# Kernel optimization log

Measured on AMD Instinct MI355X. Metric: run time of the kernel, lower is better.

Reference implementation:

```python
import jax, jax.numpy as jnp
import numpy as np

N = 50000      # nodes
E = 800000     # edges
IN = 128       # in_channels
HID = 128      # hidden_channels
OUT = 2        # out_channels (edge classes)
HEADS = 8      # EGConv default num_heads
BASES = 4      # EGConv default num_bases
FH = HID // HEADS  # per-head feature dim = 16


def _egconv(x, Wb, Wc, bc, b, row, col, norm, n):
    """One EGConv layer (aggregators=['symnorm']), self-loops already in row/col/norm.
    Wb: [in, BASES*FH] basis projection (no bias).
    Wc: [in, HEADS*BASES], bc: combination weights linear.
    b : [HID] output bias.
    """
    bases = x @ Wb                                            # [n, BASES*FH]
    msg = bases[row] * norm[:, None]                          # gather + symnorm scale
    agg = jax.ops.segment_sum(msg, col, num_segments=n)       # scatter-add -> [n, BASES*FH]
    w = (x @ Wc + bc).reshape(n, HEADS, BASES)                # per-node combination weights
    out = jnp.einsum('nhb,nbf->nhf', w, agg.reshape(n, BASES, FH))
    return out.reshape(n, HEADS * FH) + b


def setup_inputs() -> dict:
    key = jax.random.key(0)
    ks = jax.random.split(key, 12)
    s = 0.05
    inp = {
        'x': jax.random.normal(ks[0], (N, IN), jnp.float32),
        'edge_index': jax.random.randint(ks[1], (2, E), 0, N, jnp.int64),
        # conv1
        'Wb1': jax.random.normal(ks[2], (IN, BASES * FH), jnp.float32) * s,
        'Wc1': jax.random.normal(ks[3], (IN, HEADS * BASES), jnp.float32) * s,
        'bc1': jnp.zeros((HEADS * BASES,), jnp.float32),
        'b1': jnp.zeros((HID,), jnp.float32),
        # conv2
        'Wb2': jax.random.normal(ks[4], (HID, BASES * FH), jnp.float32) * s,
        'Wc2': jax.random.normal(ks[5], (HID, HEADS * BASES), jnp.float32) * s,
        'bc2': jnp.zeros((HEADS * BASES,), jnp.float32),
        'b2': jnp.zeros((HID,), jnp.float32),
        # edge classifier
        'Wcls': jax.random.normal(ks[6], (2 * HID, OUT), jnp.float32) * s,
        'bcls': jnp.zeros((OUT,), jnp.float32),
    }
    return inp


def reference(x, edge_index, Wb1, Wc1, bc1, b1, Wb2, Wc2, bc2, b2, Wcls, bcls):
    n = x.shape[0]
    # add self loops (EGConv default add_self_loops=True) + gcn_norm symnorm weights
    sl = jnp.arange(n, dtype=edge_index.dtype)
    row = jnp.concatenate([edge_index[0], sl])
    col = jnp.concatenate([edge_index[1], sl])
    deg = jax.ops.segment_sum(jnp.ones(row.shape[0], x.dtype), col, num_segments=n)
    dis = jnp.where(deg > 0, deg, 1.0) ** -0.5
    dis = jnp.where(deg > 0, dis, 0.0)
    norm = dis[row] * dis[col]                                # symnorm edge weight

    h = jax.nn.relu(_egconv(x, Wb1, Wc1, bc1, b1, row, col, norm, n))
    h = _egconv(h, Wb2, Wc2, bc2, b2, row, col, norm, n)

    # edge classifier: gather endpoint embeddings of ORIGINAL edges, concat, linear
    e = jnp.concatenate([h[edge_index[0]], h[edge_index[1]]], axis=-1)  # [E, 2*HID]
    return e @ Wcls + bcls
```

## Files before the change

kernel.cpp:

```cpp
#include <hip/hip_runtime.h>
#include <hip/hip_fp16.h>

#define NN 50000
#define EE 800000
#define NB_E2 1563
#define WIN 6250
#define EPB 1024
#define NCHUNK 782

__global__ void k_count(const int* __restrict__ ei, int* cnt, int* __restrict__ rank) {
    int t = blockIdx.x * 256 + threadIdx.x;
    if (t < EE / 2) {
        int2 cc = *(const int2*)(ei + EE + 2 * t);
        int r0 = atomicAdd(&cnt[cc.x], 1);
        int r1 = atomicAdd(&cnt[cc.y], 1);
        *(int2*)(rank + 2 * t) = make_int2(r0, r1);
    }
}

__global__ void k_scan1(const int* __restrict__ cnt, int* sloc, int* bsum,
                        float* dis, int n) {
    __shared__ int s[256];
    int tid = threadIdx.x;
    int i = blockIdx.x * 256 + tid;
    int v = (i < n) ? cnt[i] : 0;
    if (i < n) dis[i] = rsqrtf((float)v + 1.0f);
    s[tid] = v;
    __syncthreads();
    for (int off = 1; off < 256; off <<= 1) {
        int t2 = 0;
        if (tid >= off) t2 = s[tid - off];
        __syncthreads();
        if (tid >= off) s[tid] += t2;
        __syncthreads();
    }
    if (i < n) sloc[i] = s[tid] - v;
    if (tid == 255) bsum[blockIdx.x] = s[255];
}

__global__ void k_scan23(const int* __restrict__ sloc, const int* __restrict__ bsum,
                         const int* __restrict__ cnt, int2* sd, int* starts,
                         int n, int nb) {
    __shared__ int sb[256];
    int tid = threadIdx.x, b = blockIdx.x;
    int v = (tid < nb && tid < b) ? bsum[tid] : 0;
    sb[tid] = v;
    __syncthreads();
    for (int off = 128; off; off >>= 1) {
        if (tid < off) sb[tid] += sb[tid + off];
        __syncthreads();
    }
    int boff = sb[0];
    int i = b * 256 + tid;
    if (i < n) {
        int st = sloc[i] + boff;
        sd[i] = make_int2(st, cnt[i]);
        starts[i] = st;
    }
}

__global__ __launch_bounds__(256) void k_fill(
    const int* __restrict__ ei, const int* __restrict__ rank,
    const int* __restrict__ starts, int* __restrict__ csr)
{
    int w = blockIdx.x & 7;
    int chunk = blockIdx.x >> 3;
    int base = chunk * EPB + threadIdx.x * 4;
    int lo = w * WIN, hi = lo + WIN;
    if (base + 3 < EE) {
        int4 rr = *(const int4*)(ei + base);
        int4 cc = *(const int4*)(ei + EE + base);
        int4 rk = *(const int4*)(rank + base);
        if (cc.x >= lo && cc.x < hi) csr[starts[cc.x] + rk.x] = rr.x;
        if (cc.y >= lo && cc.y < hi) csr[starts[cc.y] + rk.y] = rr.y;
        if (cc.z >= lo && cc.z < hi) csr[starts[cc.z] + rk.z] = rr.z;
        if (cc.w >= lo && cc.w < hi) csr[starts[cc.w] + rk.w] = rr.w;
    } else {
        for (int e = 0; e < 4; e++) {
            int t = base + e;
            if (t < EE) {
                int c = ei[EE + t];
                if (c >= lo && c < hi) csr[starts[c] + rank[t]] = ei[t];
            }
        }
    }
}

__global__ __launch_bounds__(256) void k_gemm(
    const float* __restrict__ x, const float* __restrict__ Wb,
    const float* __restrict__ Wc, const float* __restrict__ bc,
    const float* __restrict__ dis,
    __half* __restrict__ bsh, float* __restrict__ wcomb, int n)
{
    __shared__ float xt[32 * 257];
    int tid = threadIdx.x;
    int grp = blockIdx.y;
    int row0 = blockIdx.x * 256;
    int row = row0 + tid;
    bool valid = row < n;

    const float* W = (grp < 2) ? (Wb + grp * 32) : Wc;
    const int ldw = (grp < 2) ? 64 : 32;

    float acc[32];
#pragma unroll
    for (int c = 0; c < 32; c++) acc[c] = 0.f;

    for (int s = 0; s < 4; s++) {
        int base_k = s * 32;
        float4 v[8];
#pragma unroll
        for (int i = 0; i < 8; i++) {
            int idx = i * 256 + tid;
            int r = idx >> 3;
            int k4 = idx & 7;
            int gr = row0 + r;
            v[i] = (gr < n) ? *(const float4*)(x + (size_t)gr * 128 + base_k + k4 * 4)
                            : make_float4(0.f, 0.f, 0.f, 0.f);
        }
        __syncthreads();
#pragma unroll
        for (int i = 0; i < 8; i++) {
            int idx = i * 256 + tid;
            int r = idx >> 3;
            int k4 = idx & 7;
            xt[(k4 * 4 + 0) * 257 + r] = v[i].x;
            xt[(k4 * 4 + 1) * 257 + r] = v[i].y;
            xt[(k4 * 4 + 2) * 257 + r] = v[i].z;
            xt[(k4 * 4 + 3) * 257 + r] = v[i].w;
        }
        __syncthreads();

        const float* Ws = W + base_k * ldw;
#pragma unroll 8
        for (int k = 0; k < 32; k++) {
            float xs = xt[k * 257 + tid];
            const float* wk = Ws + k * ldw;
#pragma unroll
            for (int c = 0; c < 32; c++) acc[c] = fmaf(xs, wk[c], acc[c]);
        }
    }

    if (!valid) return;
    if (grp < 2) {
        float d = dis[row];
        __half2 hh[16];
#pragma unroll
        for (int c = 0; c < 16; c++)
            hh[c] = __floats2half2_rn(acc[2 * c] * d, acc[2 * c + 1] * d);
        uint4* bo = (uint4*)(bsh + (size_t)row * 64 + grp * 32);
        const uint4* src = (const uint4*)hh;
#pragma unroll
        for (int c = 0; c < 4; c++) bo[c] = src[c];
    } else {
        float4* wo = (float4*)(wcomb + (size_t)row * 32);
#pragma unroll
        for (int c = 0; c < 8; c++)
            wo[c] = make_float4(acc[4*c] + bc[4*c], acc[4*c+1] + bc[4*c+1],
                                acc[4*c+2] + bc[4*c+2], acc[4*c+3] + bc[4*c+3]);
    }
}

template<int LAYER2>
__global__ __launch_bounds__(256) void k_agg(
    const int* __restrict__ csr, const int2* __restrict__ sd,
    const __half* __restrict__ bsh, const float* __restrict__ dis,
    const float* __restrict__ wcomb, const float* __restrict__ bias,
    float* __restrict__ h,
    const float* __restrict__ Wcls, const float* __restrict__ bcls,
    float* __restrict__ p, int n)
{
    int wid = (blockIdx.x * 256 + threadIdx.x) >> 6;
    int lane = threadIdx.x & 63;
    if (wid >= n) return;
    int2 s2 = sd[wid];
    int start = s2.x, deg = s2.y;
    int g = lane >> 4, q = lane & 15;

    const uint2* bsp = (const uint2*)bsh;
    float4 acc4 = make_float4(0.f, 0.f, 0.f, 0.f);
    if (g == 0) {
        uint2 v = bsp[(size_t)wid * 16 + q];
        float2 lo = __half22float2(*(const __half2*)&v.x);
        float2 hi = __half22float2(*(const __half2*)&v.y);
        acc4 = make_float4(lo.x, lo.y, hi.x, hi.y);
    }

    int j = 0;
    int ia = 0, ib = 0;
    if (8 <= deg) { ia = csr[start + g]; ib = csr[start + 4 + g]; }
    while (j + 8 <= deg) {
        int jn = j + 8;
        int na = 0, nb = 0;
        if (jn + 8 <= deg) { na = csr[start + jn + g]; nb = csr[start + jn + 4 + g]; }
        uint2 v0 = bsp[(size_t)ia * 16 + q];
        uint2 v1 = bsp[(size_t)ib * 16 + q];
        float2 l0 = __half22float2(*(const __half2*)&v0.x);
        float2 h0 = __half22float2(*(const __half2*)&v0.y);
        float2 l1 = __half22float2(*(const __half2*)&v1.x);
        float2 h1 = __half22float2(*(const __half2*)&v1.y);
        acc4.x += l0.x + l1.x;
        acc4.y += l0.y + l1.y;
        acc4.z += h0.x + h1.x;
        acc4.w += h0.y + h1.y;
        ia = na; ib = nb; j = jn;
    }
    int last = start + deg - 1;
    for (; j < deg; j += 4) {
        int idx = start + j + g;
        int r = csr[min(idx, last)];
        uint2 v = bsp[(size_t)r * 16 + q];
        float2 lo = __half22float2(*(const __half2*)&v.x);
        float2 hi = __half22float2(*(const __half2*)&v.y);
        float m = (j + g < deg) ? 1.f : 0.f;
        acc4.x = fmaf(lo.x, m, acc4.x);
        acc4.y = fmaf(lo.y, m, acc4.y);
        acc4.z = fmaf(hi.x, m, acc4.z);
        acc4.w = fmaf(hi.y, m, acc4.w);
    }

    acc4.x += __shfl_xor(acc4.x, 16, 64);
    acc4.y += __shfl_xor(acc4.y, 16, 64);
    acc4.z += __shfl_xor(acc4.z, 16, 64);
    acc4.w += __shfl_xor(acc4.w, 16, 64);
    acc4.x += __shfl_xor(acc4.x, 32, 64);
    acc4.y += __shfl_xor(acc4.y, 32, 64);
    acc4.z += __shfl_xor(acc4.z, 32, 64);
    acc4.w += __shfl_xor(acc4.w, 32, 64);

    float d = dis[wid];
    acc4.x *= d; acc4.y *= d; acc4.z *= d; acc4.w *= d;

    int src = lane >> 2;
    float t0 = __shfl(acc4.x, src, 64);
    float t1 = __shfl(acc4.y, src, 64);
    float t2 = __shfl(acc4.z, src, 64);
    float t3 = __shfl(acc4.w, src, 64);
    int c = lane & 3;
    float acc = (c == 0) ? t0 : (c == 1) ? t1 : (c == 2) ? t2 : t3;

    int fh = lane & 15;
    float a0 = __shfl(acc, fh, 64);
    float a1 = __shfl(acc, 16 + fh, 64);
    float a2 = __shfl(acc, 32 + fh, 64);
    float a3 = __shfl(acc, 48 + fh, 64);
    const float* wn = wcomb + (size_t)wid * 32;
    int hd = lane >> 4;
    float s1 = bias[lane];
    float s2v = bias[64 + lane];
    s1 = fmaf(wn[hd * 4 + 0], a0, s1);
    s1 = fmaf(wn[hd * 4 + 1], a1, s1);
    s1 = fmaf(wn[hd * 4 + 2], a2, s1);
    s1 = fmaf(wn[hd * 4 + 3], a3, s1);
    s2v = fmaf(wn[(4 + hd) * 4 + 0], a0, s2v);
    s2v = fmaf(wn[(4 + hd) * 4 + 1], a1, s2v);
    s2v = fmaf(wn[(4 + hd) * 4 + 2], a2, s2v);
    s2v = fmaf(wn[(4 + hd) * 4 + 3], a3, s2v);

    if (!LAYER2) {
        s1 = fmaxf(s1, 0.f);
        s2v = fmaxf(s2v, 0.f);
        h[(size_t)wid * 128 + lane] = s1;
        h[(size_t)wid * 128 + 64 + lane] = s2v;
    } else {
        float r0 = s1 * Wcls[lane * 2 + 0] + s2v * Wcls[(64 + lane) * 2 + 0];
        float r1 = s1 * Wcls[lane * 2 + 1] + s2v * Wcls[(64 + lane) * 2 + 1];
        float r2 = s1 * Wcls[(128 + lane) * 2 + 0] + s2v * Wcls[(192 + lane) * 2 + 0];
        float r3 = s1 * Wcls[(128 + lane) * 2 + 1] + s2v * Wcls[(192 + lane) * 2 + 1];
#pragma unroll
        for (int off = 32; off; off >>= 1) {
            r0 += __shfl_xor(r0, off, 64);
            r1 += __shfl_xor(r1, off, 64);
            r2 += __shfl_xor(r2, off, 64);
            r3 += __shfl_xor(r3, off, 64);
        }
        if (lane == 0) {
            p[wid * 4 + 0] = r0 + bcls[0];
            p[wid * 4 + 1] = r1 + bcls[1];
            p[wid * 4 + 2] = r2;
            p[wid * 4 + 3] = r3;
        }
    }
}

__global__ void k_edge(const int* __restrict__ ei, const float* __restrict__ p,
                       float* __restrict__ out)
{
    int t = blockIdx.x * blockDim.x + threadIdx.x;
    if (t >= EE / 2) return;
    int2 rr = *(const int2*)(ei + 2 * t);
    int2 cc = *(const int2*)(ei + EE + 2 * t);
    float2 pt0 = *(const float2*)(p + rr.x * 4);
    float2 pt1 = *(const float2*)(p + rr.y * 4);
    float2 pb0 = *(const float2*)(p + cc.x * 4 + 2);
    float2 pb1 = *(const float2*)(p + cc.y * 4 + 2);
    float4 o;
    o.x = pt0.x + pb0.x;
    o.y = pt0.y + pb0.y;
    o.z = pt1.x + pb1.x;
    o.w = pt1.y + pb1.y;
    *(float4*)(out + (size_t)t * 4) = o;
}

extern "C" void kernel_launch(void* const* d_in, const int* in_sizes, int n_in,
                              void* d_out, int out_size, void* d_ws, size_t ws_size,
                              hipStream_t stream) {
    const float* x    = (const float*)d_in[0];
    const int*   ei   = (const int*)d_in[1];
    const float* Wb1  = (const float*)d_in[2];
    const float* Wc1  = (const float*)d_in[3];
    const float* bc1  = (const float*)d_in[4];
    const float* b1   = (const float*)d_in[5];
    const float* Wb2  = (const float*)d_in[6];
    const float* Wc2  = (const float*)d_in[7];
    const float* bc2  = (const float*)d_in[8];
    const float* b2   = (const float*)d_in[9];
    const float* Wcls = (const float*)d_in[10];
    const float* bcls = (const float*)d_in[11];
    float* out = (float*)d_out;

    char* ws = (char*)d_ws;
    size_t off = 0;
    auto alloc = [&](size_t bytes) {
        void* pp = ws + off;
        off += (bytes + 15) & ~(size_t)15;
        return pp;
    };

    float*  dis    = (float*)alloc(50048 * 4);
    __half* bsh    = (__half*)alloc((size_t)NN * 64 * 2);
    float*  wcomb  = (float*)alloc((size_t)NN * 32 * 4);
    float*  h      = (float*)alloc((size_t)NN * 128 * 4);
    float*  p      = (float*)alloc((size_t)NN * 4 * 4);
    int*    cnt    = (int*)alloc(50048 * 4);
    int*    sloc   = (int*)alloc(50048 * 4);
    int*    starts = (int*)alloc(50048 * 4);
    int*    bsum   = (int*)alloc(256 * 4);
    int2*   sd     = (int2*)alloc((size_t)50048 * 8);
    int*    csr    = (int*)alloc((size_t)EE * 4);
    int*    rank   = (int*)alloc((size_t)EE * 4);

    const int B = 256;
    int gN   = (NN + B - 1) / B;
    int gN64 = (NN * 64) / B;
    dim3 gG(gN, 3);

    hipMemsetAsync(cnt, 0, NN * sizeof(int), stream);
    k_count<<<NB_E2, B, 0, stream>>>(ei, cnt, rank);
    k_scan1<<<gN, B, 0, stream>>>(cnt, sloc, bsum, dis, NN);
    k_scan23<<<gN, B, 0, stream>>>(sloc, bsum, cnt, sd, starts, NN, gN);
    k_fill<<<NCHUNK * 8, B, 0, stream>>>(ei, rank, starts, csr);

    k_gemm<<<gG, B, 0, stream>>>(x, Wb1, Wc1, bc1, dis, bsh, wcomb, NN);
    k_agg<0><<<gN64, B, 0, stream>>>(csr, sd, bsh, dis, wcomb, b1, h,
                                     Wcls, bcls, p, NN);

    k_gemm<<<gG, B, 0, stream>>>(h, Wb2, Wc2, bc2, dis, bsh, wcomb, NN);
    k_agg<1><<<gN64, B, 0, stream>>>(csr, sd, bsh, dis, wcomb, b2, h,
                                     Wcls, bcls, p, NN);

    k_edge<<<NB_E2, B, 0, stream>>>(ei, p, out);
}
```

Baseline: 278.7 us.

## Fuse CSR build into one persistent kernel with software grid barriers

Replaces the memset, count, two scan kernels and fill kernel with a single persistent kernel of 1536 blocks. The phases are separated by atomic-counter grid barriers, and the scan keeps local offsets in registers instead of a global sloc array. This is meant to remove four launch gaps and several small-kernel tails. In exchange it relies on all 1536 blocks being co-resident (launch bounds of 6 blocks per CU), or the barriers deadlock. The counters are never reset, so correctness across repeated calls depends on the modular target computation.

```diff
diff --git a/kernel.cpp b/kernel.cpp
--- a/kernel.cpp
+++ b/kernel.cpp
@@ -7,80 +7,106 @@
 #define WIN 6250
 #define EPB 1024
 #define NCHUNK 782
-
-__global__ void k_count(const int* __restrict__ ei, int* cnt, int* __restrict__ rank) {
-    int t = blockIdx.x * 256 + threadIdx.x;
-    if (t < EE / 2) {
+#define NUNIT (NCHUNK * 8)
+#define GRID_CSR 1536
+
+__device__ unsigned g_ctr[4];
+
+__device__ __forceinline__ void gridbar(unsigned* ctr) {
+    __syncthreads();
+    if (threadIdx.x == 0) {
+        __threadfence();
+        unsigned old = __hip_atomic_fetch_add(ctr, 1u, __ATOMIC_ACQ_REL,
+                                              __HIP_MEMORY_SCOPE_AGENT);
+        unsigned target = (old / GRID_CSR + 1u) * (unsigned)GRID_CSR;
+        while (__hip_atomic_load(ctr, __ATOMIC_ACQUIRE,
+                                 __HIP_MEMORY_SCOPE_AGENT) < target)
+            __builtin_amdgcn_s_sleep(1);
+        __threadfence();
+    }
+    __syncthreads();
+}
+
+__global__ __launch_bounds__(256, 6) void k_csr(
+    const int* __restrict__ ei, int* __restrict__ cnt, int* __restrict__ rank,
+    float* __restrict__ dis, int2* __restrict__ sd, int* __restrict__ starts,
+    int* __restrict__ bsum, int* __restrict__ csr)
+{
+    int b = blockIdx.x, tid = threadIdx.x;
+    __shared__ int s[256];
+    __shared__ int sb[256];
+
+    {
+        int i = b * 256 + tid;
+        if (i < NN) cnt[i] = 0;
+    }
+    gridbar(&g_ctr[0]);
+
+    for (int t = b * 256 + tid; t < EE / 2; t += GRID_CSR * 256) {
         int2 cc = *(const int2*)(ei + EE + 2 * t);
         int r0 = atomicAdd(&cnt[cc.x], 1);
         int r1 = atomicAdd(&cnt[cc.y], 1);
         *(int2*)(rank + 2 * t) = make_int2(r0, r1);
     }
-}
-
-__global__ void k_scan1(const int* __restrict__ cnt, int* sloc, int* bsum,
-                        float* dis, int n) {
-    __shared__ int s[256];
-    int tid = threadIdx.x;
-    int i = blockIdx.x * 256 + tid;
-    int v = (i < n) ? cnt[i] : 0;
-    if (i < n) dis[i] = rsqrtf((float)v + 1.0f);
-    s[tid] = v;
-    __syncthreads();
-    for (int off = 1; off < 256; off <<= 1) {
-        int t2 = 0;
-        if (tid >= off) t2 = s[tid - off];
+    gridbar(&g_ctr[1]);
+
+    int locv = 0, cntv = 0;
+    if (b < 196) {
+        int i = b * 256 + tid;
+        int v = (i < NN) ? cnt[i] : 0;
+        cntv = v;
+        if (i < NN) dis[i] = rsqrtf((float)v + 1.0f);
+        s[tid] = v;
         __syncthreads();
-        if (tid >= off) s[tid] += t2;
+        for (int off = 1; off < 256; off <<= 1) {
+            int t2 = (tid >= off) ? s[tid - off] : 0;
+            __syncthreads();
+            if (tid >= off) s[tid] += t2;
+            __syncthreads();
+        }
+        locv = s[tid] - v;
+        if (tid == 255) bsum[b] = s[255];
+    }
+    gridbar(&g_ctr[2]);
+
+    if (b < 196) {
+        int v = (tid < 196 && tid < b) ? bsum[tid] : 0;
+        sb[tid] = v;
         __syncthreads();
-    }
-    if (i < n) sloc[i] = s[tid] - v;
-    if (tid == 255) bsum[blockIdx.x] = s[255];
-}
-
-__global__ void k_scan23(const int* __restrict__ sloc, const int* __restrict__ bsum,
-                         const int* __restrict__ cnt, int2* sd, int* starts,
-                         int n, int nb) {
-    __shared__ int sb[256];
-    int tid = threadIdx.x, b = blockIdx.x;
-    int v = (tid < nb && tid < b) ? bsum[tid] : 0;
-    sb[tid] = v;
-    __syncthreads();
-    for (int off = 128; off; off >>= 1) {
-        if (tid < off) sb[tid] += sb[tid + off];
-        __syncthreads();
-    }
-    int boff = sb[0];
-    int i = b * 256 + tid;
-    if (i < n) {
-        int st = sloc[i] + boff;
-        sd[i] = make_int2(st, cnt[i]);
-        starts[i] = st;
-    }
-}
-
-__global__ __launch_bounds__(256) void k_fill(
-    const int* __restrict__ ei, const int* __restrict__ rank,
-    const int* __restrict__ starts, int* __restrict__ csr)
-{
-    int w = blockIdx.x & 7;
-    int chunk = blockIdx.x >> 3;
-    int base = chunk * EPB + threadIdx.x * 4;
-    int lo = w * WIN, hi = lo + WIN;
-    if (base + 3 < EE) {
-        int4 rr = *(const int4*)(ei + base);
-        int4 cc = *(const int4*)(ei + EE + base);
-        int4 rk = *(const int4*)(rank + base);
-        if (cc.x >= lo && cc.x < hi) csr[starts[cc.x] + rk.x] = rr.x;
-        if (cc.y >= lo && cc.y < hi) csr[starts[cc.y] + rk.y] = rr.y;
-        if (cc.z >= lo && cc.z < hi) csr[starts[cc.z] + rk.z] = rr.z;
-        if (cc.w >= lo && cc.w < hi) csr[starts[cc.w] + rk.w] = rr.w;
-    } else {
-        for (int e = 0; e < 4; e++) {
-            int t = base + e;
-            if (t < EE) {
-                int c = ei[EE + t];
-                if (c >= lo && c < hi) csr[starts[c] + rank[t]] = ei[t];
+        for (int off = 128; off; off >>= 1) {
+            if (tid < off) sb[tid] += sb[tid + off];
+            __syncthreads();
+        }
+        int boff = sb[0];
+        int i = b * 256 + tid;
+        if (i < NN) {
+            int st = locv + boff;
+            sd[i] = make_int2(st, cntv);
+            starts[i] = st;
+        }
+    }
+    gridbar(&g_ctr[3]);
+
+    for (int u = b; u < NUNIT; u += GRID_CSR) {
+        int w = u & 7;
+        int chunk = u >> 3;
+        int base = chunk * EPB + tid * 4;
+        int lo = w * WIN, hi = lo + WIN;
+        if (base + 3 < EE) {
+            int4 rr = *(const int4*)(ei + base);
+            int4 cc = *(const int4*)(ei + EE + base);
+            int4 rk = *(const int4*)(rank + base);
+            if (cc.x >= lo && cc.x < hi) csr[starts[cc.x] + rk.x] = rr.x;
+            if (cc.y >= lo && cc.y < hi) csr[starts[cc.y] + rk.y] = rr.y;
+            if (cc.z >= lo && cc.z < hi) csr[starts[cc.z] + rk.z] = rr.z;
+            if (cc.w >= lo && cc.w < hi) csr[starts[cc.w] + rk.w] = rr.w;
+        } else {
+            for (int e = 0; e < 4; e++) {
+                int t = base + e;
+                if (t < EE) {
+                    int c = ei[EE + t];
+                    if (c >= lo && c < hi) csr[starts[c] + rank[t]] = ei[t];
+                }
             }
         }
     }
@@ -333,7 +359,6 @@
     float*  h      = (float*)alloc((size_t)NN * 128 * 4);
     float*  p      = (float*)alloc((size_t)NN * 4 * 4);
     int*    cnt    = (int*)alloc(50048 * 4);
-    int*    sloc   = (int*)alloc(50048 * 4);
     int*    starts = (int*)alloc(50048 * 4);
     int*    bsum   = (int*)alloc(256 * 4);
     int2*   sd     = (int2*)alloc((size_t)50048 * 8);
@@ -345,11 +370,7 @@
     int gN64 = (NN * 64) / B;
     dim3 gG(gN, 3);
 
-    hipMemsetAsync(cnt, 0, NN * sizeof(int), stream);
-    k_count<<<NB_E2, B, 0, stream>>>(ei, cnt, rank);
-    k_scan1<<<gN, B, 0, stream>>>(cnt, sloc, bsum, dis, NN);
-    k_scan23<<<gN, B, 0, stream>>>(sloc, bsum, cnt, sd, starts, NN, gN);
-    k_fill<<<NCHUNK * 8, B, 0, stream>>>(ei, rank, starts, csr);
+    k_csr<<<GRID_CSR, B, 0, stream>>>(ei, cnt, rank, dis, sd, starts, bsum, csr);
 
     k_gemm<<<gG, B, 0, stream>>>(x, Wb1, Wc1, bc1, dis, bsh, wcomb, NN);
     k_agg<0><<<gN64, B, 0, stream>>>(csr, sd, bsh, dis, wcomb, b1, h,
```

Result: slower. 772.7 us (+177.3%).
